# Optimization experiments

Measured on AMD Instinct MI355X. Metric: run time of the kernel, lower is better.

The kernel has to match this reference:

```python
import jax, jax.numpy as jnp
import numpy as np
import math

D_MODEL = 1024
N_HEADS = 16
HEAD_DIM = D_MODEL // N_HEADS
WINDOW = 128
B, L = 1, 2048


def setup_inputs() -> dict:
    key = jax.random.key(0)
    ks = jax.random.split(key, 9)
    s = 1.0 / math.sqrt(D_MODEL)
    return {
        "hidden_states": jax.random.normal(ks[0], (B, L, D_MODEL), dtype=jnp.float32),
        "attention_mask": jnp.ones((B, L), dtype=bool),
        "Wq": jax.random.normal(ks[1], (D_MODEL, D_MODEL), dtype=jnp.float32) * s,
        "bq": jnp.zeros((D_MODEL,), dtype=jnp.float32),
        "Wk": jax.random.normal(ks[2], (D_MODEL, D_MODEL), dtype=jnp.float32) * s,
        "bk": jnp.zeros((D_MODEL,), dtype=jnp.float32),
        "Wv": jax.random.normal(ks[3], (D_MODEL, D_MODEL), dtype=jnp.float32) * s,
        "bv": jnp.zeros((D_MODEL,), dtype=jnp.float32),
        "Wo": jax.random.normal(ks[4], (D_MODEL, D_MODEL), dtype=jnp.float32) * s,
        "bo": jnp.zeros((D_MODEL,), dtype=jnp.float32),
    }


def _split_heads(x, b, l):
    # [B,L,D] -> [B,H,L,hd]
    return x.reshape(b, l, N_HEADS, HEAD_DIM).transpose(0, 2, 1, 3)


def reference(hidden_states, attention_mask, Wq, bq, Wk, bk, Wv, bv, Wo, bo):
    b, l, d = hidden_states.shape
    q = _split_heads(hidden_states @ Wq + bq, b, l)
    k = _split_heads(hidden_states @ Wk + bk, b, l)
    v = _split_heads(hidden_states @ Wv + bv, b, l)

    scale = 1.0 / math.sqrt(HEAD_DIM)
    scores = jnp.einsum("bhqd,bhkd->bhqk", q, k) * scale  # [B,H,L,L]

    # logn scaling applied to query row 0 (static: l is a compile-time shape)
    logn = math.log(max(l, 1), 512) if l > 1 else 1.0
    if logn != 1.0:
        scores = scores.at[:, :, 0, :].multiply(logn)

    # Arrow mask: row 0 attends everywhere; rows i>0 attend to |i-j|<=window plus sink col 0.
    idx = jnp.arange(l)
    band = jnp.abs(idx[:, None] - idx[None, :]) <= WINDOW       # [L,L]
    allow = band | (idx[:, None] == 0) | (idx[None, :] == 0)    # row0 + col0 full
    key_valid = attention_mask.astype(bool)                     # [B,L]
    final_allow = allow[None, :, :] & key_valid[:, None, :]     # [B,L,L]

    scores = jnp.where(final_allow[:, None, :, :], scores, -1e9)
    probs = jax.nn.softmax(scores, axis=-1)
    attn = jnp.einsum("bhqk,bhkd->bhqd", probs, v)              # [B,H,L,hd]
    out = attn.transpose(0, 2, 1, 3).reshape(b, l, d)
    return out @ Wo + bo
```

## Files before the change

### kernel.cpp

```cpp
#include <hip/hip_runtime.h>
#include <math.h>


typedef unsigned short u16;
typedef unsigned int u32;
typedef __attribute__((ext_vector_type(8))) short s16x8;
typedef __attribute__((ext_vector_type(4))) float f32x4;
typedef __attribute__((ext_vector_type(16))) float f32x16;

#define DM 1024
#define L_SEQ 2048
#define SQKV 3072

#define GLOAD16(g, l) \
  __builtin_amdgcn_global_load_lds((const __attribute__((address_space(1))) void*)(g), \
                                   (__attribute__((address_space(3))) void*)(l), 16, 0, 0)

__device__ __forceinline__ u16 f2b(float f) {
  union { float f; u32 u; } v; v.f = f;
  u32 r = v.u + 0x7fffu + ((v.u >> 16) & 1u);
  return (u16)(r >> 16);
}
__device__ __forceinline__ float b2f(u16 s) {
  union { u32 u; float f; } v; v.u = ((u32)s) << 16;
  return v.f;
}

__global__ __launch_bounds__(256) void prep_kernel(
    const float* __restrict__ hs,
    const float* __restrict__ Wq, const float* __restrict__ Wk,
    const float* __restrict__ Wv, const float* __restrict__ Wo,
    u16* __restrict__ Xb, u16* __restrict__ Wt3, u16* __restrict__ Wot) {
  __shared__ float tile[64][65];
  int bid = blockIdx.x, tid = threadIdx.x;
  if (bid < 1024) {
    int i = (bid * 256 + tid) * 8;
    float4 a = *(const float4*)(hs + i);
    float4 b = *(const float4*)(hs + i + 4);
    union { u16 t[8]; uint4 q; } u;
    u.t[0] = f2b(a.x); u.t[1] = f2b(a.y); u.t[2] = f2b(a.z); u.t[3] = f2b(a.w);
    u.t[4] = f2b(b.x); u.t[5] = f2b(b.y); u.t[6] = f2b(b.z); u.t[7] = f2b(b.w);
    *(uint4*)(Xb + i) = u.q;
  } else {
    int idx = bid - 1024;
    int z = idx >> 8, rem = idx & 255;
    int n0 = (rem & 15) * 64, k0 = (rem >> 4) * 64;
    const float* W = z == 0 ? Wq : z == 1 ? Wk : z == 2 ? Wv : Wo;
    u16* T = (z < 3) ? (Wt3 + (size_t)z * 1024 * 1024) : Wot;
    int c = tid & 63, r0 = tid >> 6;
    for (int r = r0; r < 64; r += 4) tile[r][c] = W[(size_t)(k0 + r) * DM + n0 + c];
    __syncthreads();
    for (int r = r0; r < 64; r += 4) T[(size_t)(n0 + r) * DM + k0 + c] = f2b(tile[c][r]);
  }
}

template <bool QKV>
__global__ __launch_bounds__(256) void gemm2_kernel(
    const u16* __restrict__ A, const u16* __restrict__ W,
    const float* __restrict__ bq, const float* __restrict__ bk, const float* __restrict__ bv,
    u16* __restrict__ Oq, u16* __restrict__ Vt, float* __restrict__ Of) {
  constexpr int NF32 = QKV ? 2 : 1;
  constexpr int BN = NF32 * 64;
  __shared__ u16 LB[(128 + BN) * 64];
  char* Al = (char*)LB;
  char* Bl = (char*)LB + 128 * 128;
  int m0 = blockIdx.y * 128, n0 = blockIdx.x * BN;
  int tid = threadIdx.x, lane = tid & 63, w = tid >> 6;
  int wm = w >> 1, wn = w & 1;
  f32x16 acc[2][NF32];
#pragma unroll
  for (int i = 0; i < 2; ++i)
#pragma unroll
    for (int j = 0; j < NF32; ++j)
      acc[i][j] = (f32x16){0.f,0.f,0.f,0.f,0.f,0.f,0.f,0.f,0.f,0.f,0.f,0.f,0.f,0.f,0.f,0.f};

  for (int kt = 0; kt < 16; ++kt) {
    __syncthreads();
#pragma unroll
    for (int i = 0; i < 4; ++i) {
      int u = tid + i * 256;
      int r = u >> 3, bp = u & 7;
      int off = kt * 128 + ((bp ^ (r & 7)) * 16);
      GLOAD16((const char*)A + (size_t)(m0 + r) * 2048 + off, Al + u * 16);
    }
#pragma unroll
    for (int i = 0; i < BN / 32; ++i) {
      int u = tid + i * 256;
      int r = u >> 3, bp = u & 7;
      int off = kt * 128 + ((bp ^ (r & 7)) * 16);
      GLOAD16((const char*)W + (size_t)(n0 + r) * 2048 + off, Bl + u * 16);
    }
    __syncthreads();
#pragma unroll
    for (int kk = 0; kk < 4; ++kk) {
      int bl = kk * 2 + (lane >> 5);
      s16x8 af[2], bfr[NF32];
#pragma unroll
      for (int mi = 0; mi < 2; ++mi) {
        int r = wm * 64 + mi * 32 + (lane & 31);
        af[mi] = *(const s16x8*)(Al + r * 128 + ((bl ^ (r & 7)) * 16));
      }
#pragma unroll
      for (int ni = 0; ni < NF32; ++ni) {
        int r = wn * (NF32 * 32) + ni * 32 + (lane & 31);
        bfr[ni] = *(const s16x8*)(Bl + r * 128 + ((bl ^ (r & 7)) * 16));
      }
#pragma unroll
      for (int mi = 0; mi < 2; ++mi)
#pragma unroll
        for (int ni = 0; ni < NF32; ++ni)
          acc[mi][ni] = __builtin_amdgcn_mfma_f32_32x32x16_bf16(af[mi], bfr[ni], acc[mi][ni], 0, 0, 0);
    }
  }

  const float* bias;
  if constexpr (QKV) {
    int sel = n0 >> 10;
    bias = sel == 0 ? bq : (sel == 1 ? bk : bv);
  } else {
    bias = bq;
  }
  bool isV = QKV && (n0 >= 2048);
#pragma unroll
  for (int ni = 0; ni < NF32; ++ni) {
    int col = n0 + wn * (NF32 * 32) + ni * 32 + (lane & 31);
    float bb = bias[col & 1023];
#pragma unroll
    for (int mi = 0; mi < 2; ++mi) {
      int rowb = m0 + wm * 64 + mi * 32 + 4 * (lane >> 5);
#pragma unroll
      for (int q = 0; q < 4; ++q) {
        int rb = rowb + 8 * q;
        if constexpr (QKV) {
          union { u16 t[4]; uint2 qv; } pk;
#pragma unroll
          for (int rr = 0; rr < 4; ++rr) {
            float v = acc[mi][ni][q * 4 + rr] + bb;
            u16 bvv = f2b(v);
            pk.t[rr] = bvv;
            Oq[(size_t)(rb + rr) * SQKV + col] = bvv;
          }
          if (isV) *(uint2*)(Vt + (size_t)(col - 2048) * L_SEQ + rb) = pk.qv;
        } else {
#pragma unroll
          for (int rr = 0; rr < 4; ++rr)
            Of[(size_t)(rb + rr) * DM + col] = acc[mi][ni][q * 4 + rr] + bb;
        }
      }
    }
  }
}

__global__ __launch_bounds__(256, 4) void attn_band_kernel(
    const u16* __restrict__ QKVp, const u16* __restrict__ Vt,
    u16* __restrict__ Ab, float* __restrict__ R0P) {
  int qt = blockIdx.x, h = blockIdx.y;
  __shared__ float S[32 * 308];
  __shared__ float rinv[32];
  int tid = threadIdx.x, lane = tid & 63, w = tid >> 6, g = lane >> 4;

  if (qt >= 64) {
    int kb = qt - 64;
    float* qv = S; float* wmx = S + 64; float* wsv = S + 68;
    float* pb = S + 72; float* op = S + 328;
    if (tid < 64) qv[tid] = b2f(QKVp[h * 64 + tid]);
    __syncthreads();
    const float cf = 0.125f * (11.f / 9.f);
    int j = kb * 256 + tid;
    const u16* kr = QKVp + (size_t)j * SQKV + 1024 + h * 64;
    float d = 0.f;
#pragma unroll
    for (int t8 = 0; t8 < 8; ++t8) {
      s16x8 kv8 = *(const s16x8*)(kr + t8 * 8);
#pragma unroll
      for (int e = 0; e < 8; ++e) d += qv[t8 * 8 + e] * b2f((u16)kv8[e]);
    }
    float sc = d * cf;
    float lm = sc;
#pragma unroll
    for (int dd = 1; dd < 64; dd <<= 1) lm = fmaxf(lm, __shfl_xor(lm, dd, 64));
    if (lane == 0) wmx[w] = lm;
    __syncthreads();
    float M = fmaxf(fmaxf(wmx[0], wmx[1]), fmaxf(wmx[2], wmx[3]));
    float p = __expf(sc - M);
    pb[tid] = p;
    float ls = p;
#pragma unroll
    for (int dd = 1; dd < 64; dd <<= 1) ls += __shfl_xor(ls, dd, 64);
    if (lane == 0) wsv[w] = ls;
    __syncthreads();
    float Sp = (wsv[0] + wsv[1]) + (wsv[2] + wsv[3]);
    float acc = 0.f;
    for (int t = 0; t < 64; ++t) {
      acc += pb[w * 64 + t] *
             b2f(QKVp[(size_t)(kb * 256 + w * 64 + t) * SQKV + 2048 + h * 64 + lane]);
    }
    op[w * 64 + lane] = acc;
    __syncthreads();
    float* base = R0P + (size_t)(h * 8 + kb) * 66;
    if (tid < 64) base[tid] = (op[tid] + op[64 + tid]) + (op[128 + tid] + op[192 + tid]);
    if (tid == 0) { base[64] = M; base[65] = Sp; }
    return;
  }

  int q0 = qt * 32;
  int kstart = q0 - 128; if (kstart < 0) kstart = 0;
  int kend = q0 + 32 + 128; if (kend > L_SEQ) kend = L_SEQ;
  int nsink = (kstart > 0) ? 1 : 0;
  int NCC = nsink + ((kend - kstart) >> 4);
  int NC = NCC << 4;
  const float scl = 0.125f;

  s16x8 qf[2][2];
#pragma unroll
  for (int qs = 0; qs < 2; ++qs)
#pragma unroll
    for (int kk = 0; kk < 2; ++kk)
      qf[qs][kk] = *(const s16x8*)(QKVp + (size_t)(q0 + qs * 16 + (lane & 15)) * SQKV +
                                   h * 64 + kk * 32 + g * 8);

  for (int cc = w; cc < NCC; cc += 4) {
    int keyb = (nsink && cc == 0) ? 0 : kstart + (cc - nsink) * 16;
    s16x8 kf[2];
#pragma unroll
    for (int kk = 0; kk < 2; ++kk)
      kf[kk] = *(const s16x8*)(QKVp + (size_t)(keyb + (lane & 15)) * SQKV + 1024 +
                               h * 64 + kk * 32 + g * 8);
    int colr = lane & 15;
#pragma unroll
    for (int qs = 0; qs < 2; ++qs) {
      f32x4 sa = (f32x4){0.f, 0.f, 0.f, 0.f};
      sa = __builtin_amdgcn_mfma_f32_16x16x32_bf16(qf[qs][0], kf[0], sa, 0, 0, 0);
      sa = __builtin_amdgcn_mfma_f32_16x16x32_bf16(qf[qs][1], kf[1], sa, 0, 0, 0);
#pragma unroll
      for (int ri = 0; ri < 4; ++ri) {
        int row = qs * 16 + g * 4 + ri;
        int qi = q0 + row;
        bool valid;
        if (nsink && cc == 0) {
          valid = (colr == 0);
        } else {
          int j = keyb + colr;
          int ad = qi - j; if (ad < 0) ad = -ad;
          valid = (ad <= 128) || (j == 0);
        }
        S[row * 308 + cc * 16 + colr] = valid ? sa[ri] * scl : -1e9f;
      }
    }
  }
  __syncthreads();

  {
    int row = tid >> 3, x = tid & 7;
    float* sr = S + row * 308;
    float m = -1e30f;
    for (int c = x * 4; c < NC; c += 32) {
      f32x4 v = *(const f32x4*)(sr + c);
      m = fmaxf(m, fmaxf(fmaxf(v[0], v[1]), fmaxf(v[2], v[3])));
    }
#pragma unroll
    for (int d = 1; d < 8; d <<= 1) m = fmaxf(m, __shfl_xor(m, d, 64));
    float s = 0.f;
    for (int c = x * 4; c < NC; c += 32) {
      f32x4 v = *(const f32x4*)(sr + c);
#pragma unroll
      for (int e = 0; e < 4; ++e) v[e] = __expf(v[e] - m);
      *(f32x4*)(sr + c) = v;
      s += (v[0] + v[1]) + (v[2] + v[3]);
    }
#pragma unroll
    for (int d = 1; d < 8; d <<= 1) s += __shfl_xor(s, d, 64);
    if (x == 0) rinv[row] = 1.f / s;
  }
  __syncthreads();

  {
    int qs = w & 1, db = (w >> 1) * 32;
    int NK32 = (NCC + 1) >> 1;
    f32x4 oa0 = (f32x4){0.f, 0.f, 0.f, 0.f};
    f32x4 oa1 = (f32x4){0.f, 0.f, 0.f, 0.f};
    for (int kc = 0; kc < NK32; ++kc) {
      int colb = kc * 32 + g * 8;
      union { u16 t[8]; s16x8 v; } pa;
      if (colb < NC) {
        const float* sp = &S[(qs * 16 + (lane & 15)) * 308 + colb];
        f32x4 p0 = *(const f32x4*)sp;
        f32x4 p1 = *(const f32x4*)(sp + 4);
#pragma unroll
        for (int e = 0; e < 4; ++e) { pa.t[e] = f2b(p0[e]); pa.t[4 + e] = f2b(p1[e]); }
      } else {
        pa.v = (s16x8){0, 0, 0, 0, 0, 0, 0, 0};
      }
      int keyb = (nsink && colb < 16) ? colb : (kstart + colb - nsink * 16);
      if (keyb > L_SEQ - 8) keyb = L_SEQ - 8;
      const u16* vr = Vt + (size_t)(h * 64 + db + (lane & 15)) * L_SEQ + keyb;
      s16x8 v0 = *(const s16x8*)vr;
      s16x8 v1 = *(const s16x8*)(vr + 16 * L_SEQ);
      oa0 = __builtin_amdgcn_mfma_f32_16x16x32_bf16(pa.v, v0, oa0, 0, 0, 0);
      oa1 = __builtin_amdgcn_mfma_f32_16x16x32_bf16(pa.v, v1, oa1, 0, 0, 0);
    }
#pragma unroll
    for (int ri = 0; ri < 4; ++ri) {
      int row = qs * 16 + g * 4 + ri;
      float rv = rinv[row];
      size_t base = (size_t)(q0 + row) * DM + h * 64 + db + (lane & 15);
      Ab[base] = f2b(oa0[ri] * rv);
      Ab[base + 16] = f2b(oa1[ri] * rv);
    }
  }
}

__global__ void row0_combine_kernel(const float* __restrict__ R0P, u16* __restrict__ Ab) {
  int h = blockIdx.x, t = threadIdx.x;
  float M = -1e30f;
#pragma unroll
  for (int kb = 0; kb < 8; ++kb) M = fmaxf(M, R0P[(size_t)(h * 8 + kb) * 66 + 64]);
  float tot = 0.f, o = 0.f;
#pragma unroll
  for (int kb = 0; kb < 8; ++kb) {
    const float* base = R0P + (size_t)(h * 8 + kb) * 66;
    float e = __expf(base[64] - M);
    tot += base[65] * e;
    o += base[t] * e;
  }
  Ab[h * 64 + t] = f2b(o / tot);
}

extern "C" void kernel_launch(void* const* d_in, const int* in_sizes, int n_in,
                              void* d_out, int out_size, void* d_ws, size_t ws_size,
                              hipStream_t stream) {
  const float* hs = (const float*)d_in[0];
  const float* Wq = (const float*)d_in[2];
  const float* bq = (const float*)d_in[3];
  const float* Wk = (const float*)d_in[4];
  const float* bk = (const float*)d_in[5];
  const float* Wv = (const float*)d_in[6];
  const float* bv = (const float*)d_in[7];
  const float* Wo = (const float*)d_in[8];
  const float* bo = (const float*)d_in[9];
  float* out = (float*)d_out;
  char* ws = (char*)d_ws;
  u16* Xb  = (u16*)(ws + (0ull << 20));
  u16* Wt3 = (u16*)(ws + (4ull << 20));
  u16* Wot = (u16*)(ws + (10ull << 20));
  u16* QKV = (u16*)(ws + (12ull << 20));
  u16* Vt  = (u16*)(ws + (24ull << 20));
  u16* Ab  = (u16*)(ws + (28ull << 20));
  float* R0P = (float*)(ws + (32ull << 20));

  prep_kernel<<<2048, 256, 0, stream>>>(hs, Wq, Wk, Wv, Wo, Xb, Wt3, Wot);
  gemm2_kernel<true><<<dim3(24, 16), 256, 0, stream>>>(Xb, Wt3, bq, bk, bv, QKV, Vt, nullptr);
  attn_band_kernel<<<dim3(72, 16), 256, 0, stream>>>(QKV, Vt, Ab, R0P);
  row0_combine_kernel<<<16, 64, 0, stream>>>(R0P, Ab);
  gemm2_kernel<false><<<dim3(16, 16), 256, 0, stream>>>(Ab, Wot, bo, bo, bo,
                                                        nullptr, nullptr, out);
}
```

Measured before the change: 80.06 us.

## Fuse row-0 combine into output GEMM, remap blocks per XCD, vectorize transpose

Removes the separate row0_combine launch. Each output-GEMM block with by==0 now recomputes the row-0 softmax combine into shared memory and patches A row 0 in LDS on every k-tile. It also remaps block IDs in both GEMMs and the attention kernel so neighbouring tiles land on the same XCD for L2 locality. The weight transpose in prep now uses float4 loads and ushort4 stores. The cost is redundant combine work in 16 blocks and an extra barrier per k-tile for those blocks.

```diff
diff --git a/kernel.cpp b/kernel.cpp
--- a/kernel.cpp
+++ b/kernel.cpp
@@ -47,10 +47,27 @@
     int n0 = (rem & 15) * 64, k0 = (rem >> 4) * 64;
     const float* W = z == 0 ? Wq : z == 1 ? Wk : z == 2 ? Wv : Wo;
     u16* T = (z < 3) ? (Wt3 + (size_t)z * 1024 * 1024) : Wot;
-    int c = tid & 63, r0 = tid >> 6;
-    for (int r = r0; r < 64; r += 4) tile[r][c] = W[(size_t)(k0 + r) * DM + n0 + c];
-    __syncthreads();
-    for (int r = r0; r < 64; r += 4) T[(size_t)(n0 + r) * DM + k0 + c] = f2b(tile[c][r]);
+    int c4 = tid & 15, r = tid >> 4;
+#pragma unroll
+    for (int it = 0; it < 4; ++it) {
+      int row = r + it * 16;
+      float4 v = *(const float4*)(W + (size_t)(k0 + row) * DM + n0 + c4 * 4);
+      tile[row][c4 * 4 + 0] = v.x;
+      tile[row][c4 * 4 + 1] = v.y;
+      tile[row][c4 * 4 + 2] = v.z;
+      tile[row][c4 * 4 + 3] = v.w;
+    }
+    __syncthreads();
+#pragma unroll
+    for (int it = 0; it < 4; ++it) {
+      int rr = r + it * 16;
+      ushort4 o4;
+      o4.x = f2b(tile[c4 * 4 + 0][rr]);
+      o4.y = f2b(tile[c4 * 4 + 1][rr]);
+      o4.z = f2b(tile[c4 * 4 + 2][rr]);
+      o4.w = f2b(tile[c4 * 4 + 3][rr]);
+      *(ushort4*)(T + (size_t)(n0 + rr) * DM + k0 + c4 * 4) = o4;
+    }
   }
 }
 
@@ -58,15 +75,52 @@
 __global__ __launch_bounds__(256) void gemm2_kernel(
     const u16* __restrict__ A, const u16* __restrict__ W,
     const float* __restrict__ bq, const float* __restrict__ bk, const float* __restrict__ bv,
-    u16* __restrict__ Oq, u16* __restrict__ Vt, float* __restrict__ Of) {
+    u16* __restrict__ Oq, u16* __restrict__ Vt, float* __restrict__ Of,
+    const float* __restrict__ R0P) {
   constexpr int NF32 = QKV ? 2 : 1;
   constexpr int BN = NF32 * 64;
   __shared__ u16 LB[(128 + BN) * 64];
+  __shared__ u16 Cmb[QKV ? 1 : 1024];
   char* Al = (char*)LB;
   char* Bl = (char*)LB + 128 * 128;
-  int m0 = blockIdx.y * 128, n0 = blockIdx.x * BN;
   int tid = threadIdx.x, lane = tid & 63, w = tid >> 6;
+
+  int bx, by;
+  if constexpr (QKV) {
+    int bid = blockIdx.x + 24 * blockIdx.y;
+    int c = bid & 7, local = bid >> 3;
+    bx = (c & 3) * 6 + local % 6;
+    by = (c >> 2) * 8 + local / 6;
+  } else {
+    int bid = blockIdx.x + 16 * blockIdx.y;
+    int c = bid & 7, local = bid >> 3;
+    by = c * 2 + (local >> 4);
+    bx = local & 15;
+  }
+  int m0 = by * 128, n0 = bx * BN;
   int wm = w >> 1, wn = w & 1;
+
+  if constexpr (!QKV) {
+    if (by == 0) {
+#pragma unroll
+      for (int it = 0; it < 4; ++it) {
+        int h = (tid >> 6) + it * 4, t = lane;
+        float M = -1e30f;
+#pragma unroll
+        for (int kb = 0; kb < 8; ++kb) M = fmaxf(M, R0P[(size_t)(h * 8 + kb) * 66 + 64]);
+        float tot = 0.f, o = 0.f;
+#pragma unroll
+        for (int kb = 0; kb < 8; ++kb) {
+          const float* base = R0P + (size_t)(h * 8 + kb) * 66;
+          float e = __expf(base[64] - M);
+          tot += base[65] * e;
+          o += base[t] * e;
+        }
+        Cmb[h * 64 + t] = f2b(o / tot);
+      }
+    }
+  }
+
   f32x16 acc[2][NF32];
 #pragma unroll
   for (int i = 0; i < 2; ++i)
@@ -91,6 +145,15 @@
       GLOAD16((const char*)W + (size_t)(n0 + r) * 2048 + off, Bl + u * 16);
     }
     __syncthreads();
+    if constexpr (!QKV) {
+      if (by == 0) {
+        if (tid < 8) {
+          uint4 vv = *(const uint4*)((const char*)Cmb + kt * 128 + tid * 16);
+          *(uint4*)(Al + tid * 16) = vv;
+        }
+        __syncthreads();
+      }
+    }
 #pragma unroll
     for (int kk = 0; kk < 4; ++kk) {
       int bl = kk * 2 + (lane >> 5);
@@ -154,7 +217,9 @@
 __global__ __launch_bounds__(256, 4) void attn_band_kernel(
     const u16* __restrict__ QKVp, const u16* __restrict__ Vt,
     u16* __restrict__ Ab, float* __restrict__ R0P) {
-  int qt = blockIdx.x, h = blockIdx.y;
+  int bid = blockIdx.x + 72 * blockIdx.y;
+  int nid = (bid & 7) * 144 + (bid >> 3);
+  int qt = nid % 72, h = nid / 72;
   __shared__ float S[32 * 308];
   __shared__ float rinv[32];
   int tid = threadIdx.x, lane = tid & 63, w = tid >> 6, g = lane >> 4;
@@ -308,22 +373,6 @@
       Ab[base + 16] = f2b(oa1[ri] * rv);
     }
   }
-}
-
-__global__ void row0_combine_kernel(const float* __restrict__ R0P, u16* __restrict__ Ab) {
-  int h = blockIdx.x, t = threadIdx.x;
-  float M = -1e30f;
-#pragma unroll
-  for (int kb = 0; kb < 8; ++kb) M = fmaxf(M, R0P[(size_t)(h * 8 + kb) * 66 + 64]);
-  float tot = 0.f, o = 0.f;
-#pragma unroll
-  for (int kb = 0; kb < 8; ++kb) {
-    const float* base = R0P + (size_t)(h * 8 + kb) * 66;
-    float e = __expf(base[64] - M);
-    tot += base[65] * e;
-    o += base[t] * e;
-  }
-  Ab[h * 64 + t] = f2b(o / tot);
 }
 
 extern "C" void kernel_launch(void* const* d_in, const int* in_sizes, int n_in,
@@ -349,9 +398,9 @@
   float* R0P = (float*)(ws + (32ull << 20));
 
   prep_kernel<<<2048, 256, 0, stream>>>(hs, Wq, Wk, Wv, Wo, Xb, Wt3, Wot);
-  gemm2_kernel<true><<<dim3(24, 16), 256, 0, stream>>>(Xb, Wt3, bq, bk, bv, QKV, Vt, nullptr);
+  gemm2_kernel<true><<<dim3(24, 16), 256, 0, stream>>>(Xb, Wt3, bq, bk, bv, QKV, Vt,
+                                                       nullptr, nullptr);
   attn_band_kernel<<<dim3(72, 16), 256, 0, stream>>>(QKV, Vt, Ab, R0P);
-  row0_combine_kernel<<<16, 64, 0, stream>>>(R0P, Ab);
   gemm2_kernel<false><<<dim3(16, 16), 256, 0, stream>>>(Ab, Wot, bo, bo, bo,
-                                                        nullptr, nullptr, out);
-}
+                                                        nullptr, nullptr, out, R0P);
+}
```

Result: faster. 74.30 us (-7.2%).
